# Optimization experiments

Measured on AMD Instinct MI355X. Metric: run time of the kernel, lower is better.

Reference implementation:

```python
import jax, jax.numpy as jnp
from jax import lax
import numpy as np

WINDOW_SIZE = 11
SIGMA = 1.5
C1 = 0.01 ** 2
C2 = 0.03 ** 2


def _window(channel, dtype):
    # 1D gaussian, matching torch: exp(-(x - ws//2)^2 / (2*sigma^2)), normalized
    x = jnp.arange(WINDOW_SIZE, dtype=jnp.float32) - WINDOW_SIZE // 2
    g = jnp.exp(-(x ** 2) / (2.0 * SIGMA ** 2))
    g = g / g.sum()
    w2d = jnp.outer(g, g)  # [ws, ws]
    return jnp.broadcast_to(w2d, (channel, 1, WINDOW_SIZE, WINDOW_SIZE)).astype(dtype)


def _depthwise_conv(x, window, channel):
    pad = WINDOW_SIZE // 2
    return lax.conv_general_dilated(
        x, window, window_strides=(1, 1),
        padding=[(pad, pad), (pad, pad)],
        dimension_numbers=('NCHW', 'OIHW', 'NCHW'),
        feature_group_count=channel)


def setup_inputs() -> dict:
    key = jax.random.key(0)
    k1, k2 = jax.random.split(key)
    img1 = jax.random.uniform(k1, (16, 3, 512, 512), dtype=jnp.float32)
    img2 = jax.random.uniform(k2, (16, 3, 512, 512), dtype=jnp.float32)
    return {'img1': img1, 'img2': img2}


def reference(img1, img2):
    channel = img1.shape[1]
    window = _window(channel, img1.dtype)
    conv = lambda t: _depthwise_conv(t, window, channel)

    mu1 = conv(img1)
    mu2 = conv(img2)
    mu1_sq = mu1 * mu1
    mu2_sq = mu2 * mu2
    mu1_mu2 = mu1 * mu2
    sigma1_sq = conv(img1 * img1) - mu1_sq
    sigma2_sq = conv(img2 * img2) - mu2_sq
    sigma12 = conv(img1 * img2) - mu1_mu2

    cs_map = (2.0 * sigma12 + C2) / (sigma1_sq + sigma2_sq + C2)
    ssim_map = (2.0 * mu1_mu2 + C1) / (mu1_sq + mu2_sq + C1) * cs_map
    return jnp.mean(ssim_map)  # size_average=True
```

## Files before the change

kernel.cpp:

```cpp
#include <hip/hip_runtime.h>
#include <math.h>

#define IMG_H 512
#define IMG_W 512
#define NPLANES 48
#define RAD 5
#define TAPS 11
#define CHUNK 33
#define STRIP 64
#define SBUF 80

typedef float v2f __attribute__((ext_vector_type(2)));

#define WAVE_FENCE_WAR()  __asm__ __volatile__("" ::: "memory")
#define WAVE_FENCE_RAW()  __asm__ __volatile__("s_waitcnt lgkmcnt(0)" ::: "memory")

struct GaussW { float w[TAPS]; };

__global__ __launch_bounds__(256, 4)
void ssim_main(const float* __restrict__ img1, const float* __restrict__ img2,
               double* __restrict__ sum_ws, GaussW gw) {
    __shared__ float2 srow[4][SBUF];
    __shared__ float wsum[4];

    const int tid  = threadIdx.x;
    const int wid  = tid >> 6;
    const int lane = tid & 63;
    const int c0   = blockIdx.x * (4 * STRIP) + wid * STRIP;
    const int y0   = blockIdx.y * CHUNK;
    const size_t pbase = (size_t)blockIdx.z * (IMG_H * IMG_W);
    const float* p1 = img1 + pbase;
    const float* p2 = img2 + pbase;
    float2* buf = srow[wid];

    v2f rab[TAPS], rsq[TAPS];
    float rx[TAPS];

    float pa, pb, pta, ptb;

    auto load_regs = [&](int r) {
        pa = pb = pta = ptb = 0.f;
        if (r >= 0 && r < IMG_H) {
            const float* row1 = p1 + (size_t)r * IMG_W;
            const float* row2 = p2 + (size_t)r * IMG_W;
            int col = c0 - RAD + lane;
            if (col >= 0 && col < IMG_W) { pa = row1[col]; pb = row2[col]; }
            if (lane < 2 * RAD) {
                int c2 = c0 + STRIP - RAD + lane;
                if (c2 < IMG_W) { pta = row1[c2]; ptb = row2[c2]; }
            }
        }
    };

    auto store_lds = [&]() {
        WAVE_FENCE_WAR();
        buf[lane] = make_float2(pa, pb);
        if (lane < 2 * RAD) buf[STRIP + lane] = make_float2(pta, ptb);
        WAVE_FENCE_RAW();
    };

    auto hconv = [&](int r, v2f& oab, v2f& osq, float& ox) {
        v2f aab = {0.f, 0.f}, asq = {0.f, 0.f};
        float ax = 0.f;
        if (r >= 0 && r < IMG_H) {
            #pragma unroll
            for (int d = 0; d < TAPS; ++d) {
                v2f v = *(const v2f*)&buf[lane + d];
                float w = gw.w[d];
                v2f wv = {w, w};
                aab = __builtin_elementwise_fma(wv, v, aab);
                v2f sq = v * v;
                asq = __builtin_elementwise_fma(wv, sq, asq);
                ax  = fmaf(w, v.x * v.y, ax);
            }
        }
        oab = aab; osq = asq; ox = ax;
    };

    load_regs(y0 - RAD);
    #pragma unroll
    for (int k = 0; k < TAPS - 1; ++k) {
        const int r = y0 - RAD + k;
        store_lds();
        load_regs(r + 1);
        hconv(r, rab[k], rsq[k], rx[k]);
    }

    const float C1v = 0.0001f;
    const float C2v = 0.0009f;
    float acc = 0.f;

    for (int kk = 0; kk < CHUNK; kk += TAPS) {
        #pragma unroll
        for (int j = 0; j < TAPS; ++j) {
            const int r = y0 - RAD + (TAPS - 1) + kk + j;
            store_lds();
            load_regs(r + 1);
            hconv(r, rab[(j + 10) % TAPS], rsq[(j + 10) % TAPS], rx[(j + 10) % TAPS]);

            const int y = y0 + kk + j;
            if (y < IMG_H) {
                v2f mu = {0.f, 0.f}, s2 = {0.f, 0.f};
                float sx = 0.f;
                #pragma unroll
                for (int t = 0; t < TAPS; ++t) {
                    const int s = (j + t) % TAPS;
                    float w = gw.w[t];
                    v2f wv = {w, w};
                    mu = __builtin_elementwise_fma(wv, rab[s], mu);
                    s2 = __builtin_elementwise_fma(wv, rsq[s], s2);
                    sx = fmaf(w, rx[s], sx);
                }
                float mu1 = mu.x, mu2 = mu.y;
                float mu1sq = mu1 * mu1, mu2sq = mu2 * mu2, mu12 = mu1 * mu2;
                float sg1 = s2.x - mu1sq, sg2 = s2.y - mu2sq, sg12 = sx - mu12;
                float num = (2.f * mu12 + C1v) * (2.f * sg12 + C2v);
                float den = (mu1sq + mu2sq + C1v) * (sg1 + sg2 + C2v);
                acc += num * __builtin_amdgcn_rcpf(den);
            }
        }
    }

    #pragma unroll
    for (int off = 32; off > 0; off >>= 1) acc += __shfl_down(acc, off, 64);
    if (lane == 0) wsum[wid] = acc;
    __syncthreads();
    if (tid == 0) {
        double s = (double)wsum[0] + (double)wsum[1] + (double)wsum[2] + (double)wsum[3];
        atomicAdd(sum_ws, s);
    }
}

__global__ void ssim_finalize(const double* __restrict__ sum_ws, float* __restrict__ out) {
    out[0] = (float)(sum_ws[0] * (1.0 / (double)(16.0 * 3.0 * 512.0 * 512.0)));
}

extern "C" void kernel_launch(void* const* d_in, const int* in_sizes, int n_in,
                              void* d_out, int out_size, void* d_ws, size_t ws_size,
                              hipStream_t stream) {
    const float* img1 = (const float*)d_in[0];
    const float* img2 = (const float*)d_in[1];
    float* out = (float*)d_out;
    double* ws = (double*)d_ws;

    hipMemsetAsync(ws, 0, sizeof(double), stream);

    GaussW gw;
    double g[TAPS], s = 0.0;
    for (int i = 0; i < TAPS; ++i) {
        double x = (double)(i - TAPS / 2);
        g[i] = exp(-(x * x) / (2.0 * 1.5 * 1.5));
        s += g[i];
    }
    for (int i = 0; i < TAPS; ++i) gw.w[i] = (float)(g[i] / s);

    dim3 grid(IMG_W / (4 * STRIP), (IMG_H + CHUNK - 1) / CHUNK, NPLANES);
    ssim_main<<<grid, 256, 0, stream>>>(img1, img2, ws, gw);
    ssim_finalize<<<1, 1, 0, stream>>>(ws, out);
}
```

Baseline: 152.9 us.

## Use buffer loads with OOB zeroing, fuse finalize via last-block counter

Global loads become raw buffer loads whose descriptor spans one plane, so out-of-range rows and columns return zero in hardware instead of going through branches. The row/boundary checks in the horizontal pass are dropped and offsets advance by a constant stride. The separate finalize kernel is replaced by an atomic block counter, so the last block writes the mean. Launch bounds also raise the occupancy target from 4 to 5 blocks per CU. Correctness depends on buffer OOB semantics: negative row offsets must wrap to large unsigned values and be rejected, and the sentinel offsets must likewise fall outside the descriptor range.

```diff
diff --git a/kernel.cpp b/kernel.cpp
--- a/kernel.cpp
+++ b/kernel.cpp
@@ -9,17 +9,24 @@
 #define CHUNK 33
 #define STRIP 64
 #define SBUF 80
+#define ROWB (IMG_W * 4)
+#define PLANEB (IMG_H * IMG_W * 4)
 
 typedef float v2f __attribute__((ext_vector_type(2)));
+typedef int   v4i __attribute__((ext_vector_type(4)));
+
+__device__ float
+llvm_amdgcn_raw_buffer_load_f32(v4i srsrc, int voffset, int soffset, int aux)
+    __asm("llvm.amdgcn.raw.buffer.load.f32");
 
 #define WAVE_FENCE_WAR()  __asm__ __volatile__("" ::: "memory")
 #define WAVE_FENCE_RAW()  __asm__ __volatile__("s_waitcnt lgkmcnt(0)" ::: "memory")
 
 struct GaussW { float w[TAPS]; };
 
-__global__ __launch_bounds__(256, 4)
+__global__ __launch_bounds__(256, 5)
 void ssim_main(const float* __restrict__ img1, const float* __restrict__ img2,
-               double* __restrict__ sum_ws, GaussW gw) {
+               double* __restrict__ sum_ws, float* __restrict__ out, GaussW gw) {
     __shared__ float2 srow[4][SBUF];
     __shared__ float wsum[4];
 
@@ -29,27 +36,33 @@
     const int c0   = blockIdx.x * (4 * STRIP) + wid * STRIP;
     const int y0   = blockIdx.y * CHUNK;
     const size_t pbase = (size_t)blockIdx.z * (IMG_H * IMG_W);
-    const float* p1 = img1 + pbase;
-    const float* p2 = img2 + pbase;
     float2* buf = srow[wid];
+
+    v4i srd1, srd2;
+    {
+        union { const float* p; int w[2]; } u;
+        u.p = img1 + pbase; srd1 = (v4i){u.w[0], u.w[1], PLANEB, 0x00020000};
+        u.p = img2 + pbase; srd2 = (v4i){u.w[0], u.w[1], PLANEB, 0x00020000};
+    }
+
+    const int colm = c0 - RAD + lane;
+    int vo = (y0 - RAD) * ROWB + colm * 4;
+    if (colm < 0) vo = 0x40000000;
+    const int c2 = c0 + STRIP - RAD + lane;
+    int vt = (y0 - RAD) * ROWB + c2 * 4;
+    if (lane >= 2 * RAD || c2 >= IMG_W) vt = 0x40000000;
 
     v2f rab[TAPS], rsq[TAPS];
     float rx[TAPS];
 
     float pa, pb, pta, ptb;
 
-    auto load_regs = [&](int r) {
-        pa = pb = pta = ptb = 0.f;
-        if (r >= 0 && r < IMG_H) {
-            const float* row1 = p1 + (size_t)r * IMG_W;
-            const float* row2 = p2 + (size_t)r * IMG_W;
-            int col = c0 - RAD + lane;
-            if (col >= 0 && col < IMG_W) { pa = row1[col]; pb = row2[col]; }
-            if (lane < 2 * RAD) {
-                int c2 = c0 + STRIP - RAD + lane;
-                if (c2 < IMG_W) { pta = row1[c2]; ptb = row2[c2]; }
-            }
-        }
+    auto load_regs = [&]() {
+        pa  = llvm_amdgcn_raw_buffer_load_f32(srd1, vo, 0, 0);
+        pb  = llvm_amdgcn_raw_buffer_load_f32(srd2, vo, 0, 0);
+        pta = llvm_amdgcn_raw_buffer_load_f32(srd1, vt, 0, 0);
+        ptb = llvm_amdgcn_raw_buffer_load_f32(srd2, vt, 0, 0);
+        vo += ROWB; vt += ROWB;
     };
 
     auto store_lds = [&]() {
@@ -59,31 +72,28 @@
         WAVE_FENCE_RAW();
     };
 
-    auto hconv = [&](int r, v2f& oab, v2f& osq, float& ox) {
+    auto hconv = [&](v2f& oab, v2f& osq, float& ox) {
         v2f aab = {0.f, 0.f}, asq = {0.f, 0.f};
         float ax = 0.f;
-        if (r >= 0 && r < IMG_H) {
-            #pragma unroll
-            for (int d = 0; d < TAPS; ++d) {
-                v2f v = *(const v2f*)&buf[lane + d];
-                float w = gw.w[d];
-                v2f wv = {w, w};
-                aab = __builtin_elementwise_fma(wv, v, aab);
-                v2f sq = v * v;
-                asq = __builtin_elementwise_fma(wv, sq, asq);
-                ax  = fmaf(w, v.x * v.y, ax);
-            }
+        #pragma unroll
+        for (int d = 0; d < TAPS; ++d) {
+            v2f v = *(const v2f*)&buf[lane + d];
+            float w = gw.w[d];
+            v2f wv = {w, w};
+            aab = __builtin_elementwise_fma(wv, v, aab);
+            v2f sq = v * v;
+            asq = __builtin_elementwise_fma(wv, sq, asq);
+            ax  = fmaf(w, v.x * v.y, ax);
         }
         oab = aab; osq = asq; ox = ax;
     };
 
-    load_regs(y0 - RAD);
+    load_regs();
     #pragma unroll
     for (int k = 0; k < TAPS - 1; ++k) {
-        const int r = y0 - RAD + k;
         store_lds();
-        load_regs(r + 1);
-        hconv(r, rab[k], rsq[k], rx[k]);
+        load_regs();
+        hconv(rab[k], rsq[k], rx[k]);
     }
 
     const float C1v = 0.0001f;
@@ -93,10 +103,9 @@
     for (int kk = 0; kk < CHUNK; kk += TAPS) {
         #pragma unroll
         for (int j = 0; j < TAPS; ++j) {
-            const int r = y0 - RAD + (TAPS - 1) + kk + j;
             store_lds();
-            load_regs(r + 1);
-            hconv(r, rab[(j + 10) % TAPS], rsq[(j + 10) % TAPS], rx[(j + 10) % TAPS]);
+            load_regs();
+            hconv(rab[(j + 10) % TAPS], rsq[(j + 10) % TAPS], rx[(j + 10) % TAPS]);
 
             const int y = y0 + kk + j;
             if (y < IMG_H) {
@@ -128,11 +137,15 @@
     if (tid == 0) {
         double s = (double)wsum[0] + (double)wsum[1] + (double)wsum[2] + (double)wsum[3];
         atomicAdd(sum_ws, s);
+        __threadfence();
+        unsigned* ctr = (unsigned*)(sum_ws + 1);
+        unsigned nb = gridDim.x * gridDim.y * gridDim.z;
+        if (atomicAdd(ctr, 1u) == nb - 1u) {
+            __threadfence();
+            double total = atomicAdd(sum_ws, 0.0);
+            out[0] = (float)(total * (1.0 / (16.0 * 3.0 * 512.0 * 512.0)));
+        }
     }
-}
-
-__global__ void ssim_finalize(const double* __restrict__ sum_ws, float* __restrict__ out) {
-    out[0] = (float)(sum_ws[0] * (1.0 / (double)(16.0 * 3.0 * 512.0 * 512.0)));
 }
 
 extern "C" void kernel_launch(void* const* d_in, const int* in_sizes, int n_in,
@@ -143,7 +156,7 @@
     float* out = (float*)d_out;
     double* ws = (double*)d_ws;
 
-    hipMemsetAsync(ws, 0, sizeof(double), stream);
+    hipMemsetAsync(ws, 0, 2 * sizeof(double), stream);
 
     GaussW gw;
     double g[TAPS], s = 0.0;
@@ -155,6 +168,5 @@
     for (int i = 0; i < TAPS; ++i) gw.w[i] = (float)(g[i] / s);
 
     dim3 grid(IMG_W / (4 * STRIP), (IMG_H + CHUNK - 1) / CHUNK, NPLANES);
-    ssim_main<<<grid, 256, 0, stream>>>(img1, img2, ws, gw);
-    ssim_finalize<<<1, 1, 0, stream>>>(ws, out);
+    ssim_main<<<grid, 256, 0, stream>>>(img1, img2, ws, out, gw);
 }
```

Result: slower. 307.5 us (+101.1%).

## Shrink row chunk to 16, fully unroll rows, fuse finalize via last-block counter

Applied to the files above, without the earlier changes.

Row chunk per block drops from 33 to 16, so the grid has more blocks (2x32x48) and each processes an exact multiple with no bounds check on output rows. The row loop is fully unrolled via a macro. The separate finalize kernel is removed: a global atomic counter lets the last block write the mean. Smaller chunks increase the halo recomputation overhead (10 extra rows per 16 instead of per 33) in exchange for better occupancy and load balance and one less launch.

```diff
diff --git a/kernel.cpp b/kernel.cpp
--- a/kernel.cpp
+++ b/kernel.cpp
@@ -6,7 +6,7 @@
 #define NPLANES 48
 #define RAD 5
 #define TAPS 11
-#define CHUNK 33
+#define CHUNK 16
 #define STRIP 64
 #define SBUF 80
 
@@ -19,7 +19,7 @@
 
 __global__ __launch_bounds__(256, 4)
 void ssim_main(const float* __restrict__ img1, const float* __restrict__ img2,
-               double* __restrict__ sum_ws, GaussW gw) {
+               double* __restrict__ sum_ws, float* __restrict__ out, GaussW gw) {
     __shared__ float2 srow[4][SBUF];
     __shared__ float wsum[4];
 
@@ -90,36 +90,38 @@
     const float C2v = 0.0009f;
     float acc = 0.f;
 
-    for (int kk = 0; kk < CHUNK; kk += TAPS) {
-        #pragma unroll
-        for (int j = 0; j < TAPS; ++j) {
-            const int r = y0 - RAD + (TAPS - 1) + kk + j;
-            store_lds();
-            load_regs(r + 1);
-            hconv(r, rab[(j + 10) % TAPS], rsq[(j + 10) % TAPS], rx[(j + 10) % TAPS]);
+    #define PROC_ROW(J)                                                        \
+    {                                                                          \
+        const int r = y0 + RAD + (J);         \
+        store_lds();                                                           \
+        load_regs(r + 1);                                                      \
+        hconv(r, rab[((J) + 10) % TAPS], rsq[((J) + 10) % TAPS],               \
+              rx[((J) + 10) % TAPS]);                                          \
+        v2f mu = {0.f, 0.f}, s2 = {0.f, 0.f};                                  \
+        float sx = 0.f;                                                        \
+        _Pragma("unroll")                                                      \
+        for (int t = 0; t < TAPS; ++t) {                                       \
+            const int s = ((J) + t) % TAPS;                        \
+            float w = gw.w[t];                                                 \
+            v2f wv = {w, w};                                                   \
+            mu = __builtin_elementwise_fma(wv, rab[s], mu);                    \
+            s2 = __builtin_elementwise_fma(wv, rsq[s], s2);                    \
+            sx = fmaf(w, rx[s], sx);                                           \
+        }                                                                      \
+        float mu1 = mu.x, mu2 = mu.y;                                          \
+        float mu1sq = mu1 * mu1, mu2sq = mu2 * mu2, mu12 = mu1 * mu2;          \
+        float sg1 = s2.x - mu1sq, sg2 = s2.y - mu2sq, sg12 = sx - mu12;        \
+        float num = (2.f * mu12 + C1v) * (2.f * sg12 + C2v);                   \
+        float den = (mu1sq + mu2sq + C1v) * (sg1 + sg2 + C2v);                 \
+        acc += num * __builtin_amdgcn_rcpf(den);                               \
+    }
 
-            const int y = y0 + kk + j;
-            if (y < IMG_H) {
-                v2f mu = {0.f, 0.f}, s2 = {0.f, 0.f};
-                float sx = 0.f;
-                #pragma unroll
-                for (int t = 0; t < TAPS; ++t) {
-                    const int s = (j + t) % TAPS;
-                    float w = gw.w[t];
-                    v2f wv = {w, w};
-                    mu = __builtin_elementwise_fma(wv, rab[s], mu);
-                    s2 = __builtin_elementwise_fma(wv, rsq[s], s2);
-                    sx = fmaf(w, rx[s], sx);
-                }
-                float mu1 = mu.x, mu2 = mu.y;
-                float mu1sq = mu1 * mu1, mu2sq = mu2 * mu2, mu12 = mu1 * mu2;
-                float sg1 = s2.x - mu1sq, sg2 = s2.y - mu2sq, sg12 = sx - mu12;
-                float num = (2.f * mu12 + C1v) * (2.f * sg12 + C2v);
-                float den = (mu1sq + mu2sq + C1v) * (sg1 + sg2 + C2v);
-                acc += num * __builtin_amdgcn_rcpf(den);
-            }
-        }
-    }
+    PROC_ROW(0)  PROC_ROW(1)  PROC_ROW(2)  PROC_ROW(3)
+    PROC_ROW(4)  PROC_ROW(5)  PROC_ROW(6)  PROC_ROW(7)
+    PROC_ROW(8)  PROC_ROW(9)  PROC_ROW(10) PROC_ROW(11)
+    PROC_ROW(12) PROC_ROW(13) PROC_ROW(14) PROC_ROW(15)
+
+    #undef PROC_ROW
 
     #pragma unroll
     for (int off = 32; off > 0; off >>= 1) acc += __shfl_down(acc, off, 64);
@@ -128,11 +130,15 @@
     if (tid == 0) {
         double s = (double)wsum[0] + (double)wsum[1] + (double)wsum[2] + (double)wsum[3];
         atomicAdd(sum_ws, s);
+        __threadfence();
+        unsigned* ctr = (unsigned*)(sum_ws + 1);
+        unsigned nb = gridDim.x * gridDim.y * gridDim.z;
+        if (atomicAdd(ctr, 1u) == nb - 1u) {
+            __threadfence();
+            double total = atomicAdd(sum_ws, 0.0);
+            out[0] = (float)(total * (1.0 / (16.0 * 3.0 * 512.0 * 512.0)));
+        }
     }
-}
-
-__global__ void ssim_finalize(const double* __restrict__ sum_ws, float* __restrict__ out) {
-    out[0] = (float)(sum_ws[0] * (1.0 / (double)(16.0 * 3.0 * 512.0 * 512.0)));
 }
 
 extern "C" void kernel_launch(void* const* d_in, const int* in_sizes, int n_in,
@@ -143,7 +149,7 @@
     float* out = (float*)d_out;
     double* ws = (double*)d_ws;
 
-    hipMemsetAsync(ws, 0, sizeof(double), stream);
+    hipMemsetAsync(ws, 0, 2 * sizeof(double), stream);
 
     GaussW gw;
     double g[TAPS], s = 0.0;
@@ -154,7 +160,6 @@
     }
     for (int i = 0; i < TAPS; ++i) gw.w[i] = (float)(g[i] / s);
 
-    dim3 grid(IMG_W / (4 * STRIP), (IMG_H + CHUNK - 1) / CHUNK, NPLANES);
-    ssim_main<<<grid, 256, 0, stream>>>(img1, img2, ws, gw);
-    ssim_finalize<<<1, 1, 0, stream>>>(ws, out);
+    dim3 grid(IMG_W / (4 * STRIP), IMG_H / CHUNK, NPLANES);
+    ssim_main<<<grid, 256, 0, stream>>>(img1, img2, ws, out, gw);
 }
```

New measurement: 307.0 us. +100.8%, slower.

## Merge squared sums and spill cross-product ring to LDS to raise occupancy

Applied to the files above, without the earlier changes.

Because only sigma1+sigma2 is needed, the two squared-intensity horizontal sums are combined into one scalar per row, which shrinks the register ring. The x*y cross-product ring moves from registers into a per-wave LDS buffer. Launch bounds go from 4 to 6 waves per SIMD. This lowers VGPR pressure so more waves can be resident, at the cost of an extra LDS write per row and 11 LDS reads per output pixel, plus a small change in rounding order.

```diff
diff --git a/kernel.cpp b/kernel.cpp
--- a/kernel.cpp
+++ b/kernel.cpp
@@ -17,11 +17,12 @@
 
 struct GaussW { float w[TAPS]; };
 
-__global__ __launch_bounds__(256, 4)
+__global__ __launch_bounds__(256, 6)
 void ssim_main(const float* __restrict__ img1, const float* __restrict__ img2,
                double* __restrict__ sum_ws, GaussW gw) {
     __shared__ float2 srow[4][SBUF];
-    __shared__ float wsum[4];
+    __shared__ float  srx[4][TAPS][64];
+    __shared__ float  wsum[4];
 
     const int tid  = threadIdx.x;
     const int wid  = tid >> 6;
@@ -31,10 +32,11 @@
     const size_t pbase = (size_t)blockIdx.z * (IMG_H * IMG_W);
     const float* p1 = img1 + pbase;
     const float* p2 = img2 + pbase;
-    float2* buf = srow[wid];
+    float2* buf  = srow[wid];
+    float*  bufx = &srx[wid][0][0];
 
-    v2f rab[TAPS], rsq[TAPS];
-    float rx[TAPS];
+    v2f rab[TAPS];
+    float rq[TAPS];
 
     float pa, pb, pta, ptb;
 
@@ -59,7 +61,7 @@
         WAVE_FENCE_RAW();
     };
 
-    auto hconv = [&](int r, v2f& oab, v2f& osq, float& ox) {
+    auto hconv = [&](int r, int slot, v2f& oab, float& orq) {
         v2f aab = {0.f, 0.f}, asq = {0.f, 0.f};
         float ax = 0.f;
         if (r >= 0 && r < IMG_H) {
@@ -74,7 +76,9 @@
                 ax  = fmaf(w, v.x * v.y, ax);
             }
         }
-        oab = aab; osq = asq; ox = ax;
+        oab = aab;
+        orq = asq.x + asq.y;
+        bufx[slot * 64 + lane] = ax;
     };
 
     load_regs(y0 - RAD);
@@ -83,7 +87,7 @@
         const int r = y0 - RAD + k;
         store_lds();
         load_regs(r + 1);
-        hconv(r, rab[k], rsq[k], rx[k]);
+        hconv(r, k, rab[k], rq[k]);
     }
 
     const float C1v = 0.0001f;
@@ -96,26 +100,28 @@
             const int r = y0 - RAD + (TAPS - 1) + kk + j;
             store_lds();
             load_regs(r + 1);
-            hconv(r, rab[(j + 10) % TAPS], rsq[(j + 10) % TAPS], rx[(j + 10) % TAPS]);
+            hconv(r, (j + 10) % TAPS, rab[(j + 10) % TAPS], rq[(j + 10) % TAPS]);
 
             const int y = y0 + kk + j;
             if (y < IMG_H) {
-                v2f mu = {0.f, 0.f}, s2 = {0.f, 0.f};
-                float sx = 0.f;
+                v2f mu = {0.f, 0.f};
+                float s2q = 0.f, sx = 0.f;
                 #pragma unroll
                 for (int t = 0; t < TAPS; ++t) {
                     const int s = (j + t) % TAPS;
                     float w = gw.w[t];
                     v2f wv = {w, w};
-                    mu = __builtin_elementwise_fma(wv, rab[s], mu);
-                    s2 = __builtin_elementwise_fma(wv, rsq[s], s2);
-                    sx = fmaf(w, rx[s], sx);
+                    mu  = __builtin_elementwise_fma(wv, rab[s], mu);
+                    s2q = fmaf(w, rq[s], s2q);
+                    sx  = fmaf(w, bufx[s * 64 + lane], sx);
                 }
                 float mu1 = mu.x, mu2 = mu.y;
                 float mu1sq = mu1 * mu1, mu2sq = mu2 * mu2, mu12 = mu1 * mu2;
-                float sg1 = s2.x - mu1sq, sg2 = s2.y - mu2sq, sg12 = sx - mu12;
+                float musq = mu1sq + mu2sq;
+                float sgs  = s2q - musq;
+                float sg12 = sx - mu12;
                 float num = (2.f * mu12 + C1v) * (2.f * sg12 + C2v);
-                float den = (mu1sq + mu2sq + C1v) * (sg1 + sg2 + C2v);
+                float den = (musq + C1v) * (sgs + C2v);
                 acc += num * __builtin_amdgcn_rcpf(den);
             }
         }
```

After: 153.8 us. No clear change (+0.5%).
